# Kernel optimization log

Measured on AMD Instinct MI355X. Metric: run time of the kernel, lower is better.

Reference implementation:

```python
import jax, jax.numpy as jnp
import numpy as np

NUM_LEVELS = 4
RADIUS = 4


def _avg_pool2(x):
    # 2x2 stride-2 average pool over the last two dims of a 5D array, VALID padding
    s = jax.lax.reduce_window(x, 0.0, jax.lax.add, (1, 1, 1, 2, 2), (1, 1, 1, 2, 2), 'VALID')
    return s / 4.0


def _forward(fmap1, fmap2, coords):
    B, C, Hf, Wf = fmap1.shape
    _, N, _, H, W = coords.shape
    K = 2 * RADIUS + 1

    # all-pairs correlation: (B, H1, W1, H2, W2), scaled by 1/sqrt(C)
    f1 = fmap1.reshape(B, C, Hf * Wf)
    f2 = fmap2.reshape(B, C, Hf * Wf)
    corr = jnp.einsum('bcp,bcq->bpq', f1, f2) / jnp.sqrt(jnp.asarray(C, fmap1.dtype))
    corr = corr.reshape(B, Hf, Wf, Hf, Wf)

    pyramid = [corr]
    c = corr
    for _ in range(NUM_LEVELS - 1):
        c = _avg_pool2(c)
        pyramid.append(c)

    # coords channels: 0 = x, 1 = y  ->  (B, N, H, W, 2)
    cf = jnp.moveaxis(coords, 2, -1)

    d = jnp.linspace(-RADIUS, RADIUS, K, dtype=corr.dtype)
    # matches torch.stack(torch.meshgrid(dy, dx, indexing='ij'), axis=-1)
    delta = jnp.stack(jnp.meshgrid(d, d, indexing='ij'), axis=-1)  # (K, K, 2)

    bi = jnp.arange(B)[:, None, None, None, None]
    hi = jnp.arange(H)[None, None, :, None, None]
    wi = jnp.arange(W)[None, None, None, :, None]

    outs = []
    for i, cl in enumerate(pyramid):
        h2, w2 = cl.shape[-2], cl.shape[-1]
        # sampling coords (B, N, H, W, K, K, 2)
        sc = cf[..., None, None, :] / (2.0 ** i) + delta
        # grid_sample(align_corners=True) with coords pre-clamped to [-1,1]
        # == bilinear sample with pixel coords clamped to the valid range
        x = jnp.clip(sc[..., 0], 0.0, w2 - 1)
        y = jnp.clip(sc[..., 1], 0.0, h2 - 1)
        x0 = jnp.floor(x)
        y0 = jnp.floor(y)
        fx = (x - x0).reshape(B, N, H, W, K * K)
        fy = (y - y0).reshape(B, N, H, W, K * K)
        x0i = x0.astype(jnp.int32).reshape(B, N, H, W, K * K)
        y0i = y0.astype(jnp.int32).reshape(B, N, H, W, K * K)
        x1i = jnp.minimum(x0i + 1, w2 - 1)  # weight fx is 0 at the boundary
        y1i = jnp.minimum(y0i + 1, h2 - 1)

        cl_flat = cl.reshape(B, H, W, h2 * w2)  # query grid == feature grid (H==Hf, W==Wf)

        def gather(yi, xi):
            idx = yi * w2 + xi  # (B, N, H, W, K*K)
            return cl_flat[bi, hi, wi, idx]

        v = (gather(y0i, x0i) * (1 - fy) * (1 - fx)
             + gather(y0i, x1i) * (1 - fy) * fx
             + gather(y1i, x0i) * fy * (1 - fx)
             + gather(y1i, x1i) * fy * fx)
        outs.append(v)  # (B, N, H, W, K*K)

    out = jnp.concatenate(outs, axis=-1)  # (B, N, H, W, num_levels*K*K)
    # torch: (B,N,H,W,Cc).reshape(B, N*Cc, H, W) -- a raw row-major reshape
    out = out.reshape(B, N * out.shape[-1], H, W)
    return out.astype(jnp.float32)


def setup_inputs() -> dict:
    key = jax.random.key(0)
    k1, k2, k3 = jax.random.split(key, 3)
    B, C, H, W, N = 2, 256, 64, 64, 8
    fmap1 = jax.random.normal(k1, (B, C, H, W), dtype=jnp.float32)
    fmap2 = jax.random.normal(k2, (B, C, H, W), dtype=jnp.float32)
    coords = jax.random.uniform(k3, (B, N, 2, H, W), dtype=jnp.float32) * (W - 1)
    return {"fmap1": fmap1, "fmap2": fmap2, "coords": coords}


def reference(fmap1, fmap2, coords):
    return _forward(fmap1, fmap2, coords)
```

## Files before the change

kernel.cpp:

```cpp
#include <hip/hip_runtime.h>
#include <hip/hip_bf16.h>
#include <stdint.h>

#define B_   2
#define C_   256
#define P_   4096
#define N_   8
#define OUTC 2592

typedef __bf16 bf16x8 __attribute__((ext_vector_type(8)));
typedef float floatx4 __attribute__((ext_vector_type(4)));
typedef unsigned short ushort8 __attribute__((ext_vector_type(8)));

__device__ __forceinline__ float bf2f(unsigned int u16) {
    union { unsigned int i; float f; } x; x.i = u16 << 16; return x.f;
}
__device__ __forceinline__ unsigned int f2bf(float f) {
    union { float f; unsigned int i; } x; x.f = f;
    unsigned int u = x.i + 0x7FFFu + ((x.i >> 16) & 1u);
    return u >> 16;
}

__global__ void conv_both(const float* __restrict__ in1, const float* __restrict__ in2,
                          __hip_bfloat16* __restrict__ out1, __hip_bfloat16* __restrict__ out2) {
    __shared__ float tile[32][33];
    int which = blockIdx.z >> 1;
    int b  = blockIdx.z & 1;
    const float* in = which ? in2 : in1;
    __hip_bfloat16* out = which ? out2 : out1;
    int p0 = blockIdx.x * 32;
    int c0 = blockIdx.y * 32;
    int tx = threadIdx.x;
    int ty0 = threadIdx.y;
    const float* ip = in + ((size_t)b * C_ + c0) * P_ + p0;
    for (int r = 0; r < 4; r++) {
        int ty = ty0 + r * 8;
        tile[ty][tx] = ip[(size_t)ty * P_ + tx];
    }
    __syncthreads();
    __hip_bfloat16* op = out + ((size_t)b * P_ + p0) * C_ + c0;
    for (int r = 0; r < 4; r++) {
        int ty = ty0 + r * 8;
        op[(size_t)ty * C_ + tx] = __float2bfloat16(tile[tx][ty]);
    }
}

__global__ __launch_bounds__(256) void gemm_corr(const __hip_bfloat16* __restrict__ A,
                                                 const __hip_bfloat16* __restrict__ Bm,
                                                 unsigned short* __restrict__ Cmat) {
    __shared__ __align__(16) __hip_bfloat16 lsmem[8192];
    __hip_bfloat16* lA = lsmem;
    __hip_bfloat16* lB = lsmem + 4096;
    const int id = blockIdx.x;
    const int bz = id >> 10;
    const int r_ = id & 1023;
    const int s_ = r_ >> 3;
    const int by = (r_ & 7) * 4 + (s_ >> 5);
    const int bx = s_ & 31;
    const int m0 = by * 128;
    const int n0 = bx * 128;
    const __hip_bfloat16* Ab = A  + (size_t)bz * P_ * C_;
    const __hip_bfloat16* Bb = Bm + (size_t)bz * P_ * C_;
    unsigned short* Cb = Cmat + (size_t)bz * P_ * P_;

    const int tid  = threadIdx.x;
    const int lane = tid & 63;
    const int w    = tid >> 6;
    const int wm   = w & 1, wn = w >> 1;

    floatx4 acc[4][4];
    for (int i = 0; i < 4; i++)
        for (int j = 0; j < 4; j++)
            acc[i][j] = floatx4{0.f, 0.f, 0.f, 0.f};

    const int srow = w * 16 + (lane >> 2);
    const int scol = (lane & 3) * 8;

    for (int k0 = 0; k0 < C_; k0 += 32) {
        for (int j = 0; j < 2; j++) {
            int row = j * 64 + srow;
            const __hip_bfloat16* ga = Ab + (size_t)(m0 + row) * C_ + k0 + scol;
            const __hip_bfloat16* gb = Bb + (size_t)(n0 + row) * C_ + k0 + scol;
            __hip_bfloat16* la = lA + (j * 64 + w * 16) * 32;
            __hip_bfloat16* lb = lB + (j * 64 + w * 16) * 32;
            __builtin_amdgcn_global_load_lds((const __attribute__((address_space(1))) void*)ga,
                                             (__attribute__((address_space(3))) void*)la, 16, 0, 0);
            __builtin_amdgcn_global_load_lds((const __attribute__((address_space(1))) void*)gb,
                                             (__attribute__((address_space(3))) void*)lb, 16, 0, 0);
        }
        __syncthreads();
        const int kq   = (lane >> 4) * 8;
        const int rsel = lane & 15;
        bf16x8 af[4], bfv[4];
        for (int i = 0; i < 4; i++) {
            af[i]  = *(const bf16x8*)&lA[(wm * 64 + i * 16 + rsel) * 32 + kq];
            bfv[i] = *(const bf16x8*)&lB[(wn * 64 + i * 16 + rsel) * 32 + kq];
        }
        for (int i = 0; i < 4; i++)
            for (int j = 0; j < 4; j++)
                acc[i][j] = __builtin_amdgcn_mfma_f32_16x16x32_bf16(af[i], bfv[j], acc[i][j], 0, 0, 0);
        __syncthreads();
    }
    const float scale = 0.0625f;
    unsigned short* sc = (unsigned short*)lsmem + w * (16 * 72);
    const int r16   = (lane >> 4) * 4;
    const int cbase = lane & 15;
    const int rdrow = lane >> 3;
    const int rdcol = (lane & 7) * 8;
    for (int i = 0; i < 4; i++) {
        #pragma unroll
        for (int j = 0; j < 4; j++)
            #pragma unroll
            for (int r = 0; r < 4; r++)
                sc[(r16 + r) * 72 + cbase + j * 16] = (unsigned short)f2bf(acc[i][j][r] * scale);
        ushort8 v0 = *(const ushort8*)&sc[rdrow * 72 + rdcol];
        ushort8 v1 = *(const ushort8*)&sc[(rdrow + 8) * 72 + rdcol];
        const int grow = m0 + wm * 64 + i * 16;
        const int gcol = n0 + wn * 64 + rdcol;
        *(ushort8*)&Cb[(size_t)(grow + rdrow) * P_ + gcol]     = v0;
        *(ushort8*)&Cb[(size_t)(grow + rdrow + 8) * P_ + gcol] = v1;
    }
}

__global__ __launch_bounds__(256) void sample_k(const unsigned short* __restrict__ c0,
                                                const float* __restrict__ coords,
                                                float* __restrict__ outp) {
    __shared__ unsigned short sl16[5680];
    __shared__ float cs[16];
    __shared__ float2 xt[288];
    __shared__ float2 yt[288];
    __shared__ __align__(16) unsigned int ctb[324];

    const int bp = blockIdx.x;
    const int b  = bp >> 12;
    const int p  = bp & 4095;
    const int tid = threadIdx.x;
    unsigned int* slu = (unsigned int*)sl16;

    {
        const uint4* g0 = (const uint4*)(c0 + (size_t)bp * 4096);
        for (int i = tid; i < 512; i += 256) {
            uint4 v = g0[i];
            int y = i >> 3, xh = (i & 7) * 4;
            int u = y * 33 + xh;
            slu[u] = v.x; slu[u + 1] = v.y; slu[u + 2] = v.z; slu[u + 3] = v.w;
        }
        if (tid < 16) cs[tid] = coords[(size_t)(b * 16 + tid) * 4096 + p];
    }
    __syncthreads();

    for (int t = tid; t < 1024; t += 256) {
        int y = t >> 5, x = t & 31;
        unsigned int a = slu[y * 66 + x];
        unsigned int c = slu[y * 66 + 33 + x];
        float s = 0.25f * (bf2f(a & 0xffff) + bf2f(a >> 16)
                         + bf2f(c & 0xffff) + bf2f(c >> 16));
        sl16[4224 + y * 34 + x] = (unsigned short)f2bf(s);
    }
    for (int t = tid; t < 324; t += 256) {
        if (t < 288) {
            int n = t / 36, rem = t - n * 36;
            int l = rem / 9, dd = rem - l * 9;
            int wl = 64 >> l;
            int pw   = (l == 0) ? 66 : (l == 1) ? 34 : (l == 2) ? 18 : 10;
            int base = (l == 0) ? 0  : (l == 1) ? 4224 : (l == 2) ? 5312 : 5600;
            float inv = 1.0f / (float)(1 << l);
            float mx = (float)(wl - 1);
            float cx = cs[n * 2 + 0], cy = cs[n * 2 + 1];
            float xx = fminf(fmaxf(cx * inv + (float)(dd - 4), 0.0f), mx);
            float yy = fminf(fmaxf(cy * inv + (float)(dd - 4), 0.0f), mx);
            float x0f = floorf(xx), y0f = floorf(yy);
            int x0 = (int)x0f, y0 = (int)y0f;
            int x1 = min(x0 + 1, wl - 1), y1 = min(y0 + 1, wl - 1);
            unsigned int xb = (unsigned int)x0 | ((unsigned int)x1 << 8);
            unsigned int yb = (unsigned int)(base + y0 * pw)
                            | ((unsigned int)(base + y1 * pw) << 16);
            xt[t] = make_float2(xx - x0f, __uint_as_float(xb));
            yt[t] = make_float2(yy - y0f, __uint_as_float(yb));
        }
        int c = t;
        int l = c / 81, k = c - l * 81;
        int i9 = k / 9, j9 = k - i9 * 9;
        ctb[c] = ((unsigned int)(l * 9 + i9) << 8) | (unsigned int)(l * 9 + j9);
    }
    __syncthreads();

    if (tid < 256) {
        int y = tid >> 4, x = tid & 15;
        unsigned int a = slu[2112 + 34 * y + x];
        unsigned int c = slu[2112 + 34 * y + 17 + x];
        float s = 0.25f * (bf2f(a & 0xffff) + bf2f(a >> 16)
                         + bf2f(c & 0xffff) + bf2f(c >> 16));
        sl16[5312 + y * 18 + x] = (unsigned short)f2bf(s);
    }
    __syncthreads();

    if (tid < 64) {
        int y = tid >> 3, x = tid & 7;
        unsigned int a = slu[2656 + 18 * y + x];
        unsigned int c = slu[2656 + 18 * y + 9 + x];
        float s = 0.25f * (bf2f(a & 0xffff) + bf2f(a >> 16)
                         + bf2f(c & 0xffff) + bf2f(c >> 16));
        sl16[5600 + y * 10 + x] = (unsigned short)f2bf(s);
    }
    __syncthreads();

    const size_t outbase = (size_t)b * ((size_t)N_ * P_ * 324) + (size_t)p * 324;
    for (int k = 0; k < 3; k++) {
        int iq = tid + k * 256;
        if (iq < 648) {
            int n = (iq * 6473) >> 19;
            int q = iq - n * 81;
            int cc0 = q * 4;
            const uint4 cv4 = *(const uint4*)&ctb[cc0];
            const int tb = n * 36;
            float vj[4];
            #pragma unroll
            for (int j = 0; j < 4; j++) {
                unsigned int cv = (j == 0) ? cv4.x : (j == 1) ? cv4.y : (j == 2) ? cv4.z : cv4.w;
                float2 xv = xt[tb + (cv >> 8)];
                float2 yv = yt[tb + (cv & 255)];
                unsigned int xb = __float_as_uint(xv.y);
                unsigned int yb = __float_as_uint(yv.y);
                int x0 = xb & 255, x1 = xb >> 8;
                int r0 = yb & 0xffff, r1 = yb >> 16;
                float fx = xv.x, fy = yv.x;
                float v00 = bf2f(sl16[r0 + x0]);
                float v01 = bf2f(sl16[r0 + x1]);
                float v10 = bf2f(sl16[r1 + x0]);
                float v11 = bf2f(sl16[r1 + x1]);
                float vx0 = v00 + fx * (v01 - v00);
                float vx1 = v10 + fx * (v11 - v10);
                vj[j] = vx0 + fy * (vx1 - vx0);
            }
            *(float4*)&outp[outbase + (size_t)n * (324 * 4096) + cc0] =
                make_float4(vj[0], vj[1], vj[2], vj[3]);
        }
    }
}

extern "C" void kernel_launch(void* const* d_in, const int* in_sizes, int n_in,
                              void* d_out, int out_size, void* d_ws, size_t ws_size,
                              hipStream_t stream) {
    const float* fmap1  = (const float*)d_in[0];
    const float* fmap2  = (const float*)d_in[1];
    const float* coords = (const float*)d_in[2];
    float* out = (float*)d_out;

    char* ws = (char*)d_ws;
    size_t off = 0;
    auto alloc = [&](size_t bytes) {
        void* ptr = ws + off;
        off += (bytes + 255) & ~(size_t)255;
        return ptr;
    };
    __hip_bfloat16* f1t = (__hip_bfloat16*)alloc((size_t)B_ * P_ * C_ * 2);
    __hip_bfloat16* f2t = (__hip_bfloat16*)alloc((size_t)B_ * P_ * C_ * 2);
    unsigned short* corr0 = (unsigned short*)alloc((size_t)B_ * P_ * 4096 * 2);

    conv_both<<<dim3(128, 8, 2 * B_), dim3(32, 8), 0, stream>>>(fmap1, fmap2, f1t, f2t);

    gemm_corr<<<dim3(2048), dim3(256), 0, stream>>>(f1t, f2t, corr0);

    sample_k<<<dim3(B_ * P_), dim3(256), 0, stream>>>(corr0, coords, out);
}
```

Baseline: 155.4 us.

## Double-buffer GEMM LDS tiles and store pyramid as packed bf16 neighbor pairs

The correlation GEMM now uses two LDS buffers so global-to-LDS loads for the next K chunk are issued before computing the current one, removing one barrier per iteration. The sampling kernel now stores each pyramid level as 32-bit words holding a pixel and its right neighbor. Each bilinear tap then needs two LDS reads instead of four 16-bit reads, and the x1 index is no longer computed. The cost is doubled GEMM LDS, which may reduce occupancy, and more LDS writes when building the pyramid.

New measurement: 165.5 us. 1.07x slower.

```diff
diff --git a/kernel.cpp b/kernel.cpp
--- a/kernel.cpp
+++ b/kernel.cpp
@@ -48,9 +48,7 @@
 __global__ __launch_bounds__(256) void gemm_corr(const __hip_bfloat16* __restrict__ A,
                                                  const __hip_bfloat16* __restrict__ Bm,
                                                  unsigned short* __restrict__ Cmat) {
-    __shared__ __align__(16) __hip_bfloat16 lsmem[8192];
-    __hip_bfloat16* lA = lsmem;
-    __hip_bfloat16* lB = lsmem + 4096;
+    __shared__ __align__(16) __hip_bfloat16 lsmem[16384];
     const int id = blockIdx.x;
     const int bz = id >> 10;
     const int r_ = id & 1023;
@@ -76,31 +74,46 @@
     const int srow = w * 16 + (lane >> 2);
     const int scol = (lane & 3) * 8;
 
-    for (int k0 = 0; k0 < C_; k0 += 32) {
+    auto stage = [&](int buf, int k0) {
+        __hip_bfloat16* base = lsmem + buf * 8192;
+        #pragma unroll
         for (int j = 0; j < 2; j++) {
             int row = j * 64 + srow;
             const __hip_bfloat16* ga = Ab + (size_t)(m0 + row) * C_ + k0 + scol;
             const __hip_bfloat16* gb = Bb + (size_t)(n0 + row) * C_ + k0 + scol;
-            __hip_bfloat16* la = lA + (j * 64 + w * 16) * 32;
-            __hip_bfloat16* lb = lB + (j * 64 + w * 16) * 32;
+            __hip_bfloat16* la = base + (j * 64 + w * 16) * 32;
+            __hip_bfloat16* lb = base + 4096 + (j * 64 + w * 16) * 32;
             __builtin_amdgcn_global_load_lds((const __attribute__((address_space(1))) void*)ga,
                                              (__attribute__((address_space(3))) void*)la, 16, 0, 0);
             __builtin_amdgcn_global_load_lds((const __attribute__((address_space(1))) void*)gb,
                                              (__attribute__((address_space(3))) void*)lb, 16, 0, 0);
         }
-        __syncthreads();
+    };
+
+    stage(0, 0);
+    __syncthreads();
+    int cur = 0;
+    for (int t = 0; t < 8; ++t) {
+        if (t < 7) stage(cur ^ 1, (t + 1) * 32);
+        const __hip_bfloat16* lA = lsmem + cur * 8192;
+        const __hip_bfloat16* lB = lA + 4096;
         const int kq   = (lane >> 4) * 8;
         const int rsel = lane & 15;
         bf16x8 af[4], bfv[4];
+        #pragma unroll
         for (int i = 0; i < 4; i++) {
             af[i]  = *(const bf16x8*)&lA[(wm * 64 + i * 16 + rsel) * 32 + kq];
             bfv[i] = *(const bf16x8*)&lB[(wn * 64 + i * 16 + rsel) * 32 + kq];
         }
+        #pragma unroll
         for (int i = 0; i < 4; i++)
+            #pragma unroll
             for (int j = 0; j < 4; j++)
                 acc[i][j] = __builtin_amdgcn_mfma_f32_16x16x32_bf16(af[i], bfv[j], acc[i][j], 0, 0, 0);
         __syncthreads();
-    }
+        cur ^= 1;
+    }
+
     const float scale = 0.0625f;
     unsigned short* sc = (unsigned short*)lsmem + w * (16 * 72);
     const int r16   = (lane >> 4) * 4;
@@ -125,7 +138,7 @@
 __global__ __launch_bounds__(256) void sample_k(const unsigned short* __restrict__ c0,
                                                 const float* __restrict__ coords,
                                                 float* __restrict__ outp) {
-    __shared__ unsigned short sl16[5680];
+    __shared__ __align__(16) unsigned int slp[5560];
     __shared__ float cs[16];
     __shared__ float2 xt[288];
     __shared__ float2 yt[288];
@@ -135,15 +148,24 @@
     const int b  = bp >> 12;
     const int p  = bp & 4095;
     const int tid = threadIdx.x;
-    unsigned int* slu = (unsigned int*)sl16;
+    unsigned short* p16 = (unsigned short*)slp;
 
     {
         const uint4* g0 = (const uint4*)(c0 + (size_t)bp * 4096);
         for (int i = tid; i < 512; i += 256) {
             uint4 v = g0[i];
-            int y = i >> 3, xh = (i & 7) * 4;
-            int u = y * 33 + xh;
-            slu[u] = v.x; slu[u + 1] = v.y; slu[u + 2] = v.z; slu[u + 3] = v.w;
+            int y = i >> 3, xh = (i & 7) * 8;
+            unsigned int nx = (unsigned int)__shfl_down((int)v.x, 1);
+            unsigned int vnext = (xh == 56) ? (v.w >> 16) : (nx & 0xffffu);
+            unsigned int* dst = slp + y * 65 + xh;
+            dst[0] = v.x;
+            dst[1] = (v.x >> 16) | (v.y << 16);
+            dst[2] = v.y;
+            dst[3] = (v.y >> 16) | (v.z << 16);
+            dst[4] = v.z;
+            dst[5] = (v.z >> 16) | (v.w << 16);
+            dst[6] = v.w;
+            dst[7] = (v.w >> 16) | (vnext << 16);
         }
         if (tid < 16) cs[tid] = coords[(size_t)(b * 16 + tid) * 4096 + p];
     }
@@ -151,19 +173,23 @@
 
     for (int t = tid; t < 1024; t += 256) {
         int y = t >> 5, x = t & 31;
-        unsigned int a = slu[y * 66 + x];
-        unsigned int c = slu[y * 66 + 33 + x];
+        unsigned int a = slp[(2 * y) * 65 + 2 * x];
+        unsigned int c = slp[(2 * y + 1) * 65 + 2 * x];
         float s = 0.25f * (bf2f(a & 0xffff) + bf2f(a >> 16)
                          + bf2f(c & 0xffff) + bf2f(c >> 16));
-        sl16[4224 + y * 34 + x] = (unsigned short)f2bf(s);
+        unsigned short sv = (unsigned short)f2bf(s);
+        int pi = 4160 + y * 33 + x;
+        p16[pi * 2] = sv;
+        if (x)       p16[(pi - 1) * 2 + 1] = sv;
+        if (x == 31) p16[pi * 2 + 1] = sv;
     }
     for (int t = tid; t < 324; t += 256) {
         if (t < 288) {
             int n = t / 36, rem = t - n * 36;
             int l = rem / 9, dd = rem - l * 9;
             int wl = 64 >> l;
-            int pw   = (l == 0) ? 66 : (l == 1) ? 34 : (l == 2) ? 18 : 10;
-            int base = (l == 0) ? 0  : (l == 1) ? 4224 : (l == 2) ? 5312 : 5600;
+            int pw   = (l == 0) ? 65 : (l == 1) ? 33   : (l == 2) ? 17   : 9;
+            int base = (l == 0) ? 0  : (l == 1) ? 4160 : (l == 2) ? 5216 : 5488;
             float inv = 1.0f / (float)(1 << l);
             float mx = (float)(wl - 1);
             float cx = cs[n * 2 + 0], cy = cs[n * 2 + 1];
@@ -171,11 +197,10 @@
             float yy = fminf(fmaxf(cy * inv + (float)(dd - 4), 0.0f), mx);
             float x0f = floorf(xx), y0f = floorf(yy);
             int x0 = (int)x0f, y0 = (int)y0f;
-            int x1 = min(x0 + 1, wl - 1), y1 = min(y0 + 1, wl - 1);
-            unsigned int xb = (unsigned int)x0 | ((unsigned int)x1 << 8);
+            int y1 = min(y0 + 1, wl - 1);
             unsigned int yb = (unsigned int)(base + y0 * pw)
                             | ((unsigned int)(base + y1 * pw) << 16);
-            xt[t] = make_float2(xx - x0f, __uint_as_float(xb));
+            xt[t] = make_float2(xx - x0f, __uint_as_float((unsigned int)x0));
             yt[t] = make_float2(yy - y0f, __uint_as_float(yb));
         }
         int c = t;
@@ -185,23 +210,31 @@
     }
     __syncthreads();
 
-    if (tid < 256) {
+    {
         int y = tid >> 4, x = tid & 15;
-        unsigned int a = slu[2112 + 34 * y + x];
-        unsigned int c = slu[2112 + 34 * y + 17 + x];
+        unsigned int a = slp[4160 + (2 * y) * 33 + 2 * x];
+        unsigned int c = slp[4160 + (2 * y + 1) * 33 + 2 * x];
         float s = 0.25f * (bf2f(a & 0xffff) + bf2f(a >> 16)
                          + bf2f(c & 0xffff) + bf2f(c >> 16));
-        sl16[5312 + y * 18 + x] = (unsigned short)f2bf(s);
+        unsigned short sv = (unsigned short)f2bf(s);
+        int pi = 5216 + y * 17 + x;
+        p16[pi * 2] = sv;
+        if (x)       p16[(pi - 1) * 2 + 1] = sv;
+        if (x == 15) p16[pi * 2 + 1] = sv;
     }
     __syncthreads();
 
     if (tid < 64) {
         int y = tid >> 3, x = tid & 7;
-        unsigned int a = slu[2656 + 18 * y + x];
-        unsigned int c = slu[2656 + 18 * y + 9 + x];
+        unsigned int a = slp[5216 + (2 * y) * 17 + 2 * x];
+        unsigned int c = slp[5216 + (2 * y + 1) * 17 + 2 * x];
         float s = 0.25f * (bf2f(a & 0xffff) + bf2f(a >> 16)
                          + bf2f(c & 0xffff) + bf2f(c >> 16));
-        sl16[5600 + y * 10 + x] = (unsigned short)f2bf(s);
+        unsigned short sv = (unsigned short)f2bf(s);
+        int pi = 5488 + y * 9 + x;
+        p16[pi * 2] = sv;
+        if (x)      p16[(pi - 1) * 2 + 1] = sv;
+        if (x == 7) p16[pi * 2 + 1] = sv;
     }
     __syncthreads();
 
@@ -220,15 +253,15 @@
                 unsigned int cv = (j == 0) ? cv4.x : (j == 1) ? cv4.y : (j == 2) ? cv4.z : cv4.w;
                 float2 xv = xt[tb + (cv >> 8)];
                 float2 yv = yt[tb + (cv & 255)];
-                unsigned int xb = __float_as_uint(xv.y);
+                unsigned int x0 = __float_as_uint(xv.y);
                 unsigned int yb = __float_as_uint(yv.y);
-                int x0 = xb & 255, x1 = xb >> 8;
-                int r0 = yb & 0xffff, r1 = yb >> 16;
+                unsigned int u0 = slp[(yb & 0xffff) + x0];
+                unsigned int u1 = slp[(yb >> 16) + x0];
                 float fx = xv.x, fy = yv.x;
-                float v00 = bf2f(sl16[r0 + x0]);
-                float v01 = bf2f(sl16[r0 + x1]);
-                float v10 = bf2f(sl16[r1 + x0]);
-                float v11 = bf2f(sl16[r1 + x1]);
+                float v00 = __uint_as_float(u0 << 16);
+                float v01 = __uint_as_float(u0 & 0xffff0000u);
+                float v10 = __uint_as_float(u1 << 16);
+                float v11 = __uint_as_float(u1 & 0xffff0000u);
                 float vx0 = v00 + fx * (v01 - v00);
                 float vx1 = v10 + fx * (v11 - v10);
                 vj[j] = vx0 + fy * (vx1 - vx0);
```

## Double-buffer GEMM LDS staging and widen sampler LDS stores with padded rows

Applied to the files above, without the earlier changes.

The correlation GEMM now keeps two LDS buffers and issues the global-to-LDS loads for the next K slice before the MFMAs on the current one. This removes one barrier per iteration and lets load latency overlap with compute, at the cost of twice the LDS per block. In the sampling kernel the level-0 row pitch grows from 33 to 34 words so each row is 8-byte aligned. That lets the staging writes use 64-bit stores instead of four scalar ones, and all pyramid-level offsets are shifted to match.

Measured after the change: 155.4 us. About the same (+0.0%).

```diff
diff --git a/kernel.cpp b/kernel.cpp
--- a/kernel.cpp
+++ b/kernel.cpp
@@ -11,6 +11,7 @@
 typedef __bf16 bf16x8 __attribute__((ext_vector_type(8)));
 typedef float floatx4 __attribute__((ext_vector_type(4)));
 typedef unsigned short ushort8 __attribute__((ext_vector_type(8)));
+typedef unsigned int uint2v __attribute__((ext_vector_type(2)));
 
 __device__ __forceinline__ float bf2f(unsigned int u16) {
     union { unsigned int i; float f; } x; x.i = u16 << 16; return x.f;
@@ -48,9 +49,7 @@
 __global__ __launch_bounds__(256) void gemm_corr(const __hip_bfloat16* __restrict__ A,
                                                  const __hip_bfloat16* __restrict__ Bm,
                                                  unsigned short* __restrict__ Cmat) {
-    __shared__ __align__(16) __hip_bfloat16 lsmem[8192];
-    __hip_bfloat16* lA = lsmem;
-    __hip_bfloat16* lB = lsmem + 4096;
+    __shared__ __align__(16) __hip_bfloat16 lsmem[16384];
     const int id = blockIdx.x;
     const int bz = id >> 10;
     const int r_ = id & 1023;
@@ -76,31 +75,46 @@
     const int srow = w * 16 + (lane >> 2);
     const int scol = (lane & 3) * 8;
 
-    for (int k0 = 0; k0 < C_; k0 += 32) {
+    auto stage = [&](int buf, int k0) {
+        __hip_bfloat16* base = lsmem + buf * 8192;
+        #pragma unroll
         for (int j = 0; j < 2; j++) {
             int row = j * 64 + srow;
             const __hip_bfloat16* ga = Ab + (size_t)(m0 + row) * C_ + k0 + scol;
             const __hip_bfloat16* gb = Bb + (size_t)(n0 + row) * C_ + k0 + scol;
-            __hip_bfloat16* la = lA + (j * 64 + w * 16) * 32;
-            __hip_bfloat16* lb = lB + (j * 64 + w * 16) * 32;
+            __hip_bfloat16* la = base + (j * 64 + w * 16) * 32;
+            __hip_bfloat16* lb = base + 4096 + (j * 64 + w * 16) * 32;
             __builtin_amdgcn_global_load_lds((const __attribute__((address_space(1))) void*)ga,
                                              (__attribute__((address_space(3))) void*)la, 16, 0, 0);
             __builtin_amdgcn_global_load_lds((const __attribute__((address_space(1))) void*)gb,
                                              (__attribute__((address_space(3))) void*)lb, 16, 0, 0);
         }
-        __syncthreads();
+    };
+
+    stage(0, 0);
+    __syncthreads();
+    int cur = 0;
+    for (int t = 0; t < 8; ++t) {
+        if (t < 7) stage(cur ^ 1, (t + 1) * 32);
+        const __hip_bfloat16* lA = lsmem + cur * 8192;
+        const __hip_bfloat16* lB = lA + 4096;
         const int kq   = (lane >> 4) * 8;
         const int rsel = lane & 15;
         bf16x8 af[4], bfv[4];
+        #pragma unroll
         for (int i = 0; i < 4; i++) {
             af[i]  = *(const bf16x8*)&lA[(wm * 64 + i * 16 + rsel) * 32 + kq];
             bfv[i] = *(const bf16x8*)&lB[(wn * 64 + i * 16 + rsel) * 32 + kq];
         }
+        #pragma unroll
         for (int i = 0; i < 4; i++)
+            #pragma unroll
             for (int j = 0; j < 4; j++)
                 acc[i][j] = __builtin_amdgcn_mfma_f32_16x16x32_bf16(af[i], bfv[j], acc[i][j], 0, 0, 0);
         __syncthreads();
-    }
+        cur ^= 1;
+    }
+
     const float scale = 0.0625f;
     unsigned short* sc = (unsigned short*)lsmem + w * (16 * 72);
     const int r16   = (lane >> 4) * 4;
@@ -125,7 +139,7 @@
 __global__ __launch_bounds__(256) void sample_k(const unsigned short* __restrict__ c0,
                                                 const float* __restrict__ coords,
                                                 float* __restrict__ outp) {
-    __shared__ unsigned short sl16[5680];
+    __shared__ __align__(16) unsigned short sl16[5808];
     __shared__ float cs[16];
     __shared__ float2 xt[288];
     __shared__ float2 yt[288];
@@ -141,9 +155,10 @@
         const uint4* g0 = (const uint4*)(c0 + (size_t)bp * 4096);
         for (int i = tid; i < 512; i += 256) {
             uint4 v = g0[i];
-            int y = i >> 3, xh = (i & 7) * 4;
-            int u = y * 33 + xh;
-            slu[u] = v.x; slu[u + 1] = v.y; slu[u + 2] = v.z; slu[u + 3] = v.w;
+            int y = i >> 3;
+            int u = y * 34 + (i & 7) * 4;
+            *(uint2v*)&slu[u]     = uint2v{v.x, v.y};
+            *(uint2v*)&slu[u + 2] = uint2v{v.z, v.w};
         }
         if (tid < 16) cs[tid] = coords[(size_t)(b * 16 + tid) * 4096 + p];
     }
@@ -151,19 +166,19 @@
 
     for (int t = tid; t < 1024; t += 256) {
         int y = t >> 5, x = t & 31;
-        unsigned int a = slu[y * 66 + x];
-        unsigned int c = slu[y * 66 + 33 + x];
+        unsigned int a = slu[y * 68 + x];
+        unsigned int c = slu[y * 68 + 34 + x];
         float s = 0.25f * (bf2f(a & 0xffff) + bf2f(a >> 16)
                          + bf2f(c & 0xffff) + bf2f(c >> 16));
-        sl16[4224 + y * 34 + x] = (unsigned short)f2bf(s);
+        sl16[4352 + y * 34 + x] = (unsigned short)f2bf(s);
     }
     for (int t = tid; t < 324; t += 256) {
         if (t < 288) {
             int n = t / 36, rem = t - n * 36;
             int l = rem / 9, dd = rem - l * 9;
             int wl = 64 >> l;
-            int pw   = (l == 0) ? 66 : (l == 1) ? 34 : (l == 2) ? 18 : 10;
-            int base = (l == 0) ? 0  : (l == 1) ? 4224 : (l == 2) ? 5312 : 5600;
+            int pw   = (l == 0) ? 68 : (l == 1) ? 34   : (l == 2) ? 18   : 10;
+            int base = (l == 0) ? 0  : (l == 1) ? 4352 : (l == 2) ? 5440 : 5728;
             float inv = 1.0f / (float)(1 << l);
             float mx = (float)(wl - 1);
             float cx = cs[n * 2 + 0], cy = cs[n * 2 + 1];
@@ -185,23 +200,23 @@
     }
     __syncthreads();
 
-    if (tid < 256) {
+    {
         int y = tid >> 4, x = tid & 15;
-        unsigned int a = slu[2112 + 34 * y + x];
-        unsigned int c = slu[2112 + 34 * y + 17 + x];
+        unsigned int a = slu[2176 + 34 * y + x];
+        unsigned int c = slu[2176 + 34 * y + 17 + x];
         float s = 0.25f * (bf2f(a & 0xffff) + bf2f(a >> 16)
                          + bf2f(c & 0xffff) + bf2f(c >> 16));
-        sl16[5312 + y * 18 + x] = (unsigned short)f2bf(s);
+        sl16[5440 + y * 18 + x] = (unsigned short)f2bf(s);
     }
     __syncthreads();
 
     if (tid < 64) {
         int y = tid >> 3, x = tid & 7;
-        unsigned int a = slu[2656 + 18 * y + x];
-        unsigned int c = slu[2656 + 18 * y + 9 + x];
+        unsigned int a = slu[2720 + 18 * y + x];
+        unsigned int c = slu[2720 + 18 * y + 9 + x];
         float s = 0.25f * (bf2f(a & 0xffff) + bf2f(a >> 16)
                          + bf2f(c & 0xffff) + bf2f(c >> 16));
-        sl16[5600 + y * 10 + x] = (unsigned short)f2bf(s);
+        sl16[5728 + y * 10 + x] = (unsigned short)f2bf(s);
     }
     __syncthreads();
 
```
